# Performance work log

Hardware: AMD Instinct MI355X
Metric: run time of the kernel (lower is better)

## Reference

```python
import jax, jax.numpy as jnp
from jax import lax
import numpy as np

RATE = 6.0          # self.rate buffer
STRIDE = 1
PAD = 1
DIL = 1
R_BLUR = 2          # gaussian blur radius for sigma=1.0 (5x5 kernel)


def _unit_circle():
    # 3x3 kernel taps: center (0,0), 8 outer taps normalized to the unit circle. (y, x) order.
    pts = []
    for ky in (-1.0, 0.0, 1.0):
        for kx in (-1.0, 0.0, 1.0):
            n = np.hypot(ky, kx)
            pts.append([ky / n, kx / n] if n > 0 else [0.0, 0.0])
    return jnp.asarray(np.array(pts, np.float32))  # (9, 2)

UNIT_CIRCLE = _unit_circle()


def blur2d_sphere(x, sigma):
    # Isotropic gaussian blur, depthwise, SAME padding. Kernel values depend on traced sigma.
    c = jnp.arange(-R_BLUR, R_BLUR + 1, dtype=x.dtype)
    g = jnp.exp(-(c[:, None] ** 2 + c[None, :] ** 2) / (2.0 * sigma * sigma))
    g = g / g.sum()
    C = x.shape[1]
    k = jnp.broadcast_to(g[None, None], (C, 1, 2 * R_BLUR + 1, 2 * R_BLUR + 1))
    return lax.conv_general_dilated(x, k, (1, 1), [(R_BLUR, R_BLUR)] * 2,
                                    feature_group_count=C)


def _axis_sample(x, pos, axis, size):
    # 1D linear interpolation gather along `axis` at fractional positions `pos`;
    # out-of-range corners contribute zero (deform_conv semantics).
    dt = x.dtype
    p0 = jnp.floor(pos)
    t = (pos - p0).astype(dt)
    i0 = p0.astype(jnp.int32)
    i1 = i0 + 1
    w0 = (1.0 - t) * ((i0 >= 0) & (i0 < size)).astype(dt)
    w1 = t * ((i1 >= 0) & (i1 < size)).astype(dt)
    g0 = jnp.take(x, jnp.clip(i0, 0, size - 1), axis=axis)
    g1 = jnp.take(x, jnp.clip(i1, 0, size - 1), axis=axis)
    sh = [1, 1, 1, 1]
    sh[axis] = -1
    return w0.reshape(sh) * g0 + w1.reshape(sh) * g1


def _forward(x, sigma, weight):
    x = blur2d_sphere(x, sigma)
    B, C, H, W = x.shape
    O = weight.shape[0]
    off = UNIT_CIRCLE.astype(x.dtype) * (sigma * RATE)  # (9, 2): per-tap (dy, dx), constant over b,h,w
    Ho = (H + 2 * PAD - DIL * 2 - 1) // STRIDE + 1
    Wo = (W + 2 * PAD - DIL * 2 - 1) // STRIDE + 1
    base_y = jnp.arange(Ho, dtype=x.dtype) * STRIDE - PAD
    base_x = jnp.arange(Wo, dtype=x.dtype) * STRIDE - PAD
    wflat = weight.reshape(O, C, 9)
    out = jnp.zeros((B, O, Ho, Wo), x.dtype)
    # Offsets are spatially constant, so deformable bilinear sampling is separable per tap.
    for ky in range(3):
        for kx in range(3):
            k = ky * 3 + kx
            py = base_y + (ky * DIL) + off[k, 0]   # (Ho,)
            px = base_x + (kx * DIL) + off[k, 1]   # (Wo,)
            xr = _axis_sample(x, py, 2, H)          # (B, C, Ho, W)
            v = _axis_sample(xr, px, 3, W)          # (B, C, Ho, Wo)
            out = out + jnp.einsum('bchw,oc->bohw', v, wflat[:, :, k])
    return out


def setup_inputs() -> dict:
    key = jax.random.key(0)
    k1, k2 = jax.random.split(key)
    x = jax.random.normal(k1, (16, 32, 256, 256), jnp.float32)
    fan_in = 32 * 9
    fan_out = 32 * 9
    limit = float(np.sqrt(6.0 / (fan_in + fan_out)))  # xavier_uniform
    weight = jax.random.uniform(k2, (32, 32, 3, 3), jnp.float32, -limit, limit)
    sigma = jnp.float32(1.0)
    return {"x": x, "sigma": sigma, "weight": weight}


def reference(x, sigma, weight):
    return _forward(x, sigma, weight)
```

## Files before the change

kernel.cpp:

```cpp
#include <hip/hip_runtime.h>
#include <math.h>

#define BB 16
#define CC 32
#define OO 32
#define HH 256
#define WW 256
#define HW (HH * WW)
#define PD 8
#define HP (HH + 2 * PD)
#define WP (WW + 2 * PD)
#define NEMAX 36

#define WROWS 30
#define WCOLS 80
#define PLANE (WROWS * WCOLS + 1)

typedef __attribute__((ext_vector_type(8))) short bf16x8;
typedef __attribute__((ext_vector_type(4))) float f32x4;
typedef __attribute__((ext_vector_type(4))) unsigned short us4;
typedef __attribute__((ext_vector_type(8))) unsigned short us8;

__device__ __forceinline__ unsigned short f2bf(float f) {
    unsigned u = __float_as_uint(f);
    u += 0x7fffu + ((u >> 16) & 1u);
    return (unsigned short)(u >> 16);
}
__device__ __forceinline__ float bf2f(unsigned short v) {
    return __uint_as_float((unsigned)v << 16);
}

__global__ __launch_bounds__(256) void blur_t_kernel(const float* __restrict__ x,
                                                     const float* __restrict__ sigma_p,
                                                     unsigned short* __restrict__ xbt) {
    __shared__ __align__(16) unsigned short vb[16][4][264];
    const int t   = threadIdx.x;
    const int blk = ((blockIdx.x & 7) << 7) + (blockIdx.x >> 3);
    const int band = blk & 63;
    const int b    = blk >> 6;
    const int h0   = band << 2;

    const float sigma = sigma_p[0];
    const float inv2s2 = 1.0f / (2.0f * sigma * sigma);
    float e[5], s = 0.0f;
#pragma unroll
    for (int i = 0; i < 5; ++i) {
        float d = (float)(i - 2);
        e[i] = expf(-(d * d) * inv2s2);
        s += e[i];
    }
    const float inv_s = 1.0f / s;
    float wn[5];
#pragma unroll
    for (int i = 0; i < 5; ++i) wn[i] = e[i] * inv_s;

    unsigned short* xb_img = xbt + (size_t)b * (HP * WP * CC);

    const us8 z8 = {0, 0, 0, 0, 0, 0, 0, 0};
    {
        const int j  = t >> 6;
        const int px = (t >> 2) & 15;
        const int ch = t & 3;
        const int xx = (px < PD) ? px : px + WW;
        *reinterpret_cast<us8*>(xb_img + ((size_t)(h0 + PD + j) * WP + xx) * CC + ch * 8) = z8;
    }
    if (h0 < PD) {
#pragma unroll
        for (int j2 = 0; j2 < 4; ++j2) {
            unsigned short* dst = xb_img + (size_t)(h0 + j2) * WP * CC;
            for (int i = t; i < (WP * CC) / 8; i += 256)
                *reinterpret_cast<us8*>(dst + i * 8) = z8;
        }
    }
    if (h0 + 4 > HH - PD) {
#pragma unroll
        for (int j2 = 0; j2 < 4; ++j2) {
            unsigned short* dst = xb_img + (size_t)(h0 + j2 + 2 * PD) * WP * CC;
            for (int i = t; i < (WP * CC) / 8; i += 256)
                *reinterpret_cast<us8*>(dst + i * 8) = z8;
        }
    }

    const int g  = t & 63;
    const int cs = t >> 6;

#pragma unroll
    for (int pass = 0; pass < 2; ++pass) {
        if (pass) __syncthreads();

        {
            const int c15 = t >> 4;
            const int j   = (t >> 2) & 3;
            const int e_  = t & 3;
            const int idx = (e_ < 2) ? (2 + e_) : (258 + e_);
            vb[c15][j][idx] = 0;
        }

#pragma unroll
        for (int it = 0; it < 4; ++it) {
            const int c = (pass << 4) + (it << 2) + cs;
            const float* xc = x + ((size_t)(b * CC + c) * HH) * WW + 4 * g;
            f32x4 v[8];
#pragma unroll
            for (int k = 0; k < 8; ++k) {
                const int r = h0 - 2 + k;
                v[k] = (r >= 0 && r < HH)
                     ? __builtin_nontemporal_load(reinterpret_cast<const f32x4*>(xc + r * WW))
                     : (f32x4){0.f, 0.f, 0.f, 0.f};
            }
#pragma unroll
            for (int j = 0; j < 4; ++j) {
                f32x4 a = {0.f, 0.f, 0.f, 0.f};
#pragma unroll
                for (int i = 0; i < 5; ++i) {
                    a[0] = fmaf(wn[i], v[j + i][0], a[0]);
                    a[1] = fmaf(wn[i], v[j + i][1], a[1]);
                    a[2] = fmaf(wn[i], v[j + i][2], a[2]);
                    a[3] = fmaf(wn[i], v[j + i][3], a[3]);
                }
                us4 bv;
                bv[0] = f2bf(a[0]); bv[1] = f2bf(a[1]);
                bv[2] = f2bf(a[2]); bv[3] = f2bf(a[3]);
                *reinterpret_cast<us4*>(&vb[c & 15][j][4 + 4 * g]) = bv;
            }
        }
        __syncthreads();

        const int cu8 = t & 1;
        const int p4  = (t >> 1) & 63;
        const int jh  = t >> 7;
        const int P   = p4 << 2;
        const int cl0 = cu8 << 3;

#pragma unroll
        for (int jj = 0; jj < 2; ++jj) {
            const int j = (jh << 1) + jj;
            us8 o[4];
#pragma unroll
            for (int cc = 0; cc < 8; ++cc) {
                const unsigned short* vp = &vb[cl0 + cc][j][P];
                us4 r0 = *reinterpret_cast<const us4*>(vp);
                us4 r1 = *reinterpret_cast<const us4*>(vp + 4);
                us4 r2 = *reinterpret_cast<const us4*>(vp + 8);
                float v[12];
#pragma unroll
                for (int q = 0; q < 4; ++q) {
                    v[q]     = bf2f(r0[q]);
                    v[4 + q] = bf2f(r1[q]);
                    v[8 + q] = bf2f(r2[q]);
                }
#pragma unroll
                for (int d = 0; d < 4; ++d) {
                    float a = 0.0f;
#pragma unroll
                    for (int i = 0; i < 5; ++i) a = fmaf(wn[i], v[d + 2 + i], a);
                    o[d][cc] = f2bf(a);
                }
            }
            unsigned short* obj = xb_img + ((size_t)(h0 + PD + j) * WP + PD + P) * CC
                                         + (pass << 4) + cl0;
#pragma unroll
            for (int d = 0; d < 4; ++d)
                *reinterpret_cast<us8*>(obj + d * CC) = o[d];
        }
    }
}

__global__ void wtrans_kernel(const float* __restrict__ wgt,
                              const float* __restrict__ sigma_p,
                              int* __restrict__ meta,
                              unsigned short* __restrict__ wb2) {
    __shared__ int   s_tap[36];
    __shared__ float s_w[36];
    __shared__ int   s_soff[36];
    __shared__ int   s_wrel[36];
    __shared__ int   s_n;
    const int t = threadIdx.x;

    if (t == 0) {
        const float UY[9] = {-0.70710678f, -1.0f, -0.70710678f, 0.0f, 0.0f, 0.0f,
                              0.70710678f,  1.0f,  0.70710678f};
        const float UX[9] = {-0.70710678f, 0.0f, 0.70710678f, -1.0f, 0.0f, 1.0f,
                             -0.70710678f, 0.0f, 0.70710678f};
        const int KYI[9] = {-1, -1, -1, 0, 0, 0, 1, 1, 1};
        const int KXI[9] = {-1, 0, 1, -1, 0, 1, -1, 0, 1};
        const float s6 = sigma_p[0] * 6.0f;
        int n = 0, ok = 1;
        for (int s_ = 0; s_ < 9; ++s_) {
            float offy = UY[s_] * s6, offx = UX[s_] * s6;
            float fy = floorf(offy), fx = floorf(offx);
            float ty = offy - fy,    tx = offx - fx;
            int sy = KYI[s_] + (int)fy;
            int sx = KXI[s_] + (int)fx;
            float wy[2] = {1.0f - ty, ty};
            float wx[2] = {1.0f - tx, tx};
            for (int dy = 0; dy < 2; ++dy)
                for (int dx = 0; dx < 2; ++dx) {
                    float wc = wy[dy] * wx[dx];
                    if (wc != 0.0f) {
                        const int syc = sy + dy, sxc = sx + dx;
                        s_tap[n]  = s_;
                        s_w[n]    = wc;
                        s_soff[n] = (syc * WP + sxc) * CC;
                        s_wrel[n] = (syc + 7) * WCOLS + (sxc + 8);
                        if (syc < -7 || syc > 7 || sxc < -7 || sxc > 7) ok = 0;
                        ++n;
                    }
                }
        }
        for (int i = 1; i < n; ++i) {
            int ks = s_soff[i]; int kt = s_tap[i]; float kw = s_w[i]; int kr = s_wrel[i];
            int j = i - 1;
            while (j >= 0 && s_soff[j] > ks) {
                s_soff[j + 1] = s_soff[j]; s_tap[j + 1] = s_tap[j];
                s_w[j + 1] = s_w[j];       s_wrel[j + 1] = s_wrel[j];
                --j;
            }
            s_soff[j + 1] = ks; s_tap[j + 1] = kt; s_w[j + 1] = kw; s_wrel[j + 1] = kr;
        }
        if (blockIdx.x == 0) {
            meta[0] = n;
            for (int i = 0; i < n; ++i) { meta[1 + i] = s_soff[i]; meta[37 + i] = s_wrel[i]; }
            meta[74] = ok;
        }
        s_n = n;
    }
    __syncthreads();

    const int e = blockIdx.x;
    if (e >= s_n) return;
    for (int i = t; i < 1024; i += 256) {
        int j  = i & 7;
        int l  = (i >> 3) & 63;
        int nh = (i >> 9) & 1;
        int o  = nh * 16 + (l & 15);
        int c  = ((l >> 4) << 3) + j;
        wb2[e * 1024 + i] = f2bf(s_w[e] * wgt[(o * CC + c) * 9 + s_tap[e]]);
    }
}

__global__ __launch_bounds__(512) void mix8_kernel(const unsigned short* __restrict__ xbt,
                                                   const int* __restrict__ meta,
                                                   const unsigned short* __restrict__ wb2,
                                                   float* __restrict__ out) {
    __shared__ bf16x8 win[4 * PLANE];
    const int t    = threadIdx.x;
    const int lane = t & 63;
    const int wv   = t >> 6;
    const int blk  = ((blockIdx.x & 7) << 7) + (blockIdx.x >> 3);
    const int xs   = blk & 3;
    const int band = (blk >> 2) & 15;
    const int b    = blk >> 6;
    const int h0   = band << 4;
    const int x0   = xs << 6;
    const int mrow = lane & 15;
    const int cu   = lane >> 4;
    const int ncorn = meta[0];
    const int ok    = meta[74];

    const unsigned short* img = xbt + (size_t)b * (HP * WP * CC);

    f32x4 acc[8][2];
#pragma unroll
    for (int q = 0; q < 8; ++q) {
        acc[q][0] = (f32x4){0.f, 0.f, 0.f, 0.f};
        acc[q][1] = (f32x4){0.f, 0.f, 0.f, 0.f};
    }

    if (ok) {
        const unsigned short* gsrc = img + ((size_t)(h0 + 1) * WP + x0) * CC;
        for (int i = t; i < WROWS * WCOLS * 4; i += 512) {
            const int cui = i & 3;
            const int pxl = (i >> 2) % WCOLS;
            const int row = (i >> 2) / WCOLS;
            win[cui * PLANE + row * WCOLS + pxl] =
                *reinterpret_cast<const bf16x8*>(gsrc + ((size_t)row * WP + pxl) * CC + cui * 8);
        }
        __syncthreads();

        const int ubase = cu * PLANE + (wv * 2) * WCOLS + mrow;
        for (int e = 0; e < ncorn; ++e) {
            const int ewr = meta[37 + e];
            const bf16x8 b0 = *reinterpret_cast<const bf16x8*>(wb2 + ((e * 2 + 0) * 64 + lane) * 8);
            const bf16x8 b1 = *reinterpret_cast<const bf16x8*>(wb2 + ((e * 2 + 1) * 64 + lane) * 8);
            const int abase = ubase + ewr;
#pragma unroll
            for (int ri = 0; ri < 2; ++ri) {
#pragma unroll
                for (int tx = 0; tx < 4; ++tx) {
                    const bf16x8 a = win[abase + ri * WCOLS + tx * 16];
                    acc[ri * 4 + tx][0] = __builtin_amdgcn_mfma_f32_16x16x32_bf16(a, b0, acc[ri * 4 + tx][0], 0, 0, 0);
                    acc[ri * 4 + tx][1] = __builtin_amdgcn_mfma_f32_16x16x32_bf16(a, b1, acc[ri * 4 + tx][1], 0, 0, 0);
                }
            }
        }
    } else {
        const unsigned short* gb = img + ((size_t)(h0 + wv * 2 + PD) * WP + x0 + PD) * CC
                                       + mrow * CC + cu * 8;
        for (int e = 0; e < ncorn; ++e) {
            const int soff = meta[1 + e];
            const bf16x8 b0 = *reinterpret_cast<const bf16x8*>(wb2 + ((e * 2 + 0) * 64 + lane) * 8);
            const bf16x8 b1 = *reinterpret_cast<const bf16x8*>(wb2 + ((e * 2 + 1) * 64 + lane) * 8);
#pragma unroll
            for (int ri = 0; ri < 2; ++ri) {
#pragma unroll
                for (int tx = 0; tx < 4; ++tx) {
                    const bf16x8 a = *reinterpret_cast<const bf16x8*>(
                        gb + soff + ((size_t)ri * WP + tx * 16) * CC);
                    acc[ri * 4 + tx][0] = __builtin_amdgcn_mfma_f32_16x16x32_bf16(a, b0, acc[ri * 4 + tx][0], 0, 0, 0);
                    acc[ri * 4 + tx][1] = __builtin_amdgcn_mfma_f32_16x16x32_bf16(a, b1, acc[ri * 4 + tx][1], 0, 0, 0);
                }
            }
        }
    }

    const int prow = cu << 2;
    float* op0 = out + ((size_t)b * OO + (lane & 15)) * HW;
#pragma unroll
    for (int ri = 0; ri < 2; ++ri) {
        float* opr = op0 + (size_t)(h0 + wv * 2 + ri) * WW + x0 + prow;
#pragma unroll
        for (int tx = 0; tx < 4; ++tx) {
            *reinterpret_cast<f32x4*>(opr + tx * 16) = acc[ri * 4 + tx][0];
            *reinterpret_cast<f32x4*>(opr + tx * 16 + (size_t)16 * HW) = acc[ri * 4 + tx][1];
        }
    }
}

extern "C" void kernel_launch(void* const* d_in, const int* in_sizes, int n_in,
                              void* d_out, int out_size, void* d_ws, size_t ws_size,
                              hipStream_t stream) {
    const float* x     = (const float*)d_in[0];
    const float* sigma = (const float*)d_in[1];
    const float* wgt   = (const float*)d_in[2];
    float* out = (float*)d_out;

    int* meta           = (int*)d_ws;
    unsigned short* wb2 = (unsigned short*)((char*)d_ws + 512);
    unsigned short* xbt = (unsigned short*)((char*)d_ws + 131072);

    wtrans_kernel<<<36, 256, 0, stream>>>(wgt, sigma, meta, wb2);
    blur_t_kernel<<<BB * 64, 256, 0, stream>>>(x, sigma, xbt);
    mix8_kernel<<<BB * 64, 512, 0, stream>>>(xbt, meta, wb2, out);
}
```

Measured before the change: 156.5 us.

## Fuse blur into the MFMA mixing kernel via shared-memory halo window

Adds a fused kernel that computes the separable 5x5 gaussian blur directly from fp32 input into the shared-memory bf16 window, then runs the MFMA tap accumulation. This skips writing and re-reading the padded bf16 intermediate image in global memory when the offsets fit in the window. The blur is recomputed over halo regions, and the old blur and mix kernels stay as a fallback that exits early on the fast path. The cost is redundant halo blur work and extra launches that return immediately.

```diff
diff --git a/kernel.cpp b/kernel.cpp
--- a/kernel.cpp
+++ b/kernel.cpp
@@ -30,16 +30,7 @@
     return __uint_as_float((unsigned)v << 16);
 }
 
-__global__ __launch_bounds__(256) void blur_t_kernel(const float* __restrict__ x,
-                                                     const float* __restrict__ sigma_p,
-                                                     unsigned short* __restrict__ xbt) {
-    __shared__ __align__(16) unsigned short vb[16][4][264];
-    const int t   = threadIdx.x;
-    const int blk = ((blockIdx.x & 7) << 7) + (blockIdx.x >> 3);
-    const int band = blk & 63;
-    const int b    = blk >> 6;
-    const int h0   = band << 2;
-
+__device__ __forceinline__ void blur_wn(const float* sigma_p, float* wn) {
     const float sigma = sigma_p[0];
     const float inv2s2 = 1.0f / (2.0f * sigma * sigma);
     float e[5], s = 0.0f;
@@ -50,120 +41,8 @@
         s += e[i];
     }
     const float inv_s = 1.0f / s;
-    float wn[5];
 #pragma unroll
     for (int i = 0; i < 5; ++i) wn[i] = e[i] * inv_s;
-
-    unsigned short* xb_img = xbt + (size_t)b * (HP * WP * CC);
-
-    const us8 z8 = {0, 0, 0, 0, 0, 0, 0, 0};
-    {
-        const int j  = t >> 6;
-        const int px = (t >> 2) & 15;
-        const int ch = t & 3;
-        const int xx = (px < PD) ? px : px + WW;
-        *reinterpret_cast<us8*>(xb_img + ((size_t)(h0 + PD + j) * WP + xx) * CC + ch * 8) = z8;
-    }
-    if (h0 < PD) {
-#pragma unroll
-        for (int j2 = 0; j2 < 4; ++j2) {
-            unsigned short* dst = xb_img + (size_t)(h0 + j2) * WP * CC;
-            for (int i = t; i < (WP * CC) / 8; i += 256)
-                *reinterpret_cast<us8*>(dst + i * 8) = z8;
-        }
-    }
-    if (h0 + 4 > HH - PD) {
-#pragma unroll
-        for (int j2 = 0; j2 < 4; ++j2) {
-            unsigned short* dst = xb_img + (size_t)(h0 + j2 + 2 * PD) * WP * CC;
-            for (int i = t; i < (WP * CC) / 8; i += 256)
-                *reinterpret_cast<us8*>(dst + i * 8) = z8;
-        }
-    }
-
-    const int g  = t & 63;
-    const int cs = t >> 6;
-
-#pragma unroll
-    for (int pass = 0; pass < 2; ++pass) {
-        if (pass) __syncthreads();
-
-        {
-            const int c15 = t >> 4;
-            const int j   = (t >> 2) & 3;
-            const int e_  = t & 3;
-            const int idx = (e_ < 2) ? (2 + e_) : (258 + e_);
-            vb[c15][j][idx] = 0;
-        }
-
-#pragma unroll
-        for (int it = 0; it < 4; ++it) {
-            const int c = (pass << 4) + (it << 2) + cs;
-            const float* xc = x + ((size_t)(b * CC + c) * HH) * WW + 4 * g;
-            f32x4 v[8];
-#pragma unroll
-            for (int k = 0; k < 8; ++k) {
-                const int r = h0 - 2 + k;
-                v[k] = (r >= 0 && r < HH)
-                     ? __builtin_nontemporal_load(reinterpret_cast<const f32x4*>(xc + r * WW))
-                     : (f32x4){0.f, 0.f, 0.f, 0.f};
-            }
-#pragma unroll
-            for (int j = 0; j < 4; ++j) {
-                f32x4 a = {0.f, 0.f, 0.f, 0.f};
-#pragma unroll
-                for (int i = 0; i < 5; ++i) {
-                    a[0] = fmaf(wn[i], v[j + i][0], a[0]);
-                    a[1] = fmaf(wn[i], v[j + i][1], a[1]);
-                    a[2] = fmaf(wn[i], v[j + i][2], a[2]);
-                    a[3] = fmaf(wn[i], v[j + i][3], a[3]);
-                }
-                us4 bv;
-                bv[0] = f2bf(a[0]); bv[1] = f2bf(a[1]);
-                bv[2] = f2bf(a[2]); bv[3] = f2bf(a[3]);
-                *reinterpret_cast<us4*>(&vb[c & 15][j][4 + 4 * g]) = bv;
-            }
-        }
-        __syncthreads();
-
-        const int cu8 = t & 1;
-        const int p4  = (t >> 1) & 63;
-        const int jh  = t >> 7;
-        const int P   = p4 << 2;
-        const int cl0 = cu8 << 3;
-
-#pragma unroll
-        for (int jj = 0; jj < 2; ++jj) {
-            const int j = (jh << 1) + jj;
-            us8 o[4];
-#pragma unroll
-            for (int cc = 0; cc < 8; ++cc) {
-                const unsigned short* vp = &vb[cl0 + cc][j][P];
-                us4 r0 = *reinterpret_cast<const us4*>(vp);
-                us4 r1 = *reinterpret_cast<const us4*>(vp + 4);
-                us4 r2 = *reinterpret_cast<const us4*>(vp + 8);
-                float v[12];
-#pragma unroll
-                for (int q = 0; q < 4; ++q) {
-                    v[q]     = bf2f(r0[q]);
-                    v[4 + q] = bf2f(r1[q]);
-                    v[8 + q] = bf2f(r2[q]);
-                }
-#pragma unroll
-                for (int d = 0; d < 4; ++d) {
-                    float a = 0.0f;
-#pragma unroll
-                    for (int i = 0; i < 5; ++i) a = fmaf(wn[i], v[d + 2 + i], a);
-                    o[d][cc] = f2bf(a);
-                }
-            }
-            unsigned short* obj = xb_img + ((size_t)(h0 + PD + j) * WP + PD + P) * CC
-                                         + (pass << 4) + cl0;
-#pragma unroll
-            for (int d = 0; d < 4; ++d)
-                *reinterpret_cast<us8*>(obj + d * CC) = o[d];
-        }
-    }
 }
 
 __global__ void wtrans_kernel(const float* __restrict__ wgt,
@@ -239,11 +118,263 @@
     }
 }
 
-__global__ __launch_bounds__(512) void mix8_kernel(const unsigned short* __restrict__ xbt,
-                                                   const int* __restrict__ meta,
-                                                   const unsigned short* __restrict__ wb2,
-                                                   float* __restrict__ out) {
+__global__ __launch_bounds__(512) void fused_kernel(const float* __restrict__ x,
+                                                    const float* __restrict__ sigma_p,
+                                                    const int* __restrict__ meta,
+                                                    const unsigned short* __restrict__ wb2,
+                                                    float* __restrict__ out) {
     __shared__ bf16x8 win[4 * PLANE];
+    if (!meta[74]) return;
+
+    const int t    = threadIdx.x;
+    const int lane = t & 63;
+    const int wv   = t >> 6;
+    const int blk  = ((blockIdx.x & 7) << 7) + (blockIdx.x >> 3);
+    const int xs   = blk & 3;
+    const int band = (blk >> 2) & 15;
+    const int b    = blk >> 6;
+    const int h0   = band << 4;
+    const int x0   = xs << 6;
+
+    float wn[5];
+    blur_wn(sigma_p, wn);
+
+    for (int tile = t; tile < 1920; tile += 512) {
+        const int c  = tile & 31;
+        const int q  = tile >> 5;
+        const int pg = q % 10;
+        const int rg = q / 10;
+
+        const int yb = h0 - 9 + rg * 5;
+        const int xa = x0 - 12 + pg * 8;
+        const float* xcp = x + ((size_t)(b * CC + c) * HH) * WW;
+
+        f32x4 a5[5][4];
+#pragma unroll
+        for (int j = 0; j < 5; ++j)
+#pragma unroll
+            for (int i = 0; i < 4; ++i) a5[j][i] = (f32x4){0.f, 0.f, 0.f, 0.f};
+
+#pragma unroll
+        for (int r = 0; r < 9; ++r) {
+            const int y = yb + r;
+            const bool rok = (y >= 0) && (y < HH);
+            const float* rp = xcp + y * WW;
+            f32x4 v[4];
+#pragma unroll
+            for (int i = 0; i < 4; ++i) {
+                const int pxb = xa + 4 * i;
+                v[i] = (rok && pxb >= 0 && pxb <= WW - 4)
+                     ? *reinterpret_cast<const f32x4*>(rp + pxb)
+                     : (f32x4){0.f, 0.f, 0.f, 0.f};
+            }
+            const int jlo = (r - 4 > 0) ? r - 4 : 0;
+            const int jhi = (r < 4) ? r : 4;
+#pragma unroll
+            for (int j = 0; j < 5; ++j) {
+                if (j < jlo || j > jhi) continue;
+                const float w = wn[r - j];
+#pragma unroll
+                for (int i = 0; i < 4; ++i) {
+                    a5[j][i][0] = fmaf(w, v[i][0], a5[j][i][0]);
+                    a5[j][i][1] = fmaf(w, v[i][1], a5[j][i][1]);
+                    a5[j][i][2] = fmaf(w, v[i][2], a5[j][i][2]);
+                    a5[j][i][3] = fmaf(w, v[i][3], a5[j][i][3]);
+                }
+            }
+        }
+
+        unsigned short* wp16 = reinterpret_cast<unsigned short*>(win)
+                             + ((c >> 3) * PLANE + (rg * 5) * WCOLS + pg * 8) * 8 + (c & 7);
+#pragma unroll
+        for (int j = 0; j < 5; ++j) {
+            const int yout = h0 - 7 + rg * 5 + j;
+            const bool row_ok = (yout >= 0) && (yout < HH);
+            float vl[16];
+#pragma unroll
+            for (int k = 0; k < 16; ++k) vl[k] = a5[j][k >> 2][k & 3];
+            unsigned short* wrow = wp16 + j * (WCOLS * 8);
+#pragma unroll
+            for (int d = 0; d < 8; ++d) {
+                const int pxo = x0 - 8 + pg * 8 + d;
+                const bool col_ok = (pxo >= 0) && (pxo < WW);
+                float o = 0.0f;
+#pragma unroll
+                for (int i = 0; i < 5; ++i) o = fmaf(wn[i], vl[2 + d + i], o);
+                wrow[d * 8] = (row_ok && col_ok) ? f2bf(o) : (unsigned short)0;
+            }
+        }
+    }
+    __syncthreads();
+
+    const int mrow = lane & 15;
+    const int cu   = lane >> 4;
+    const int ncorn = meta[0];
+
+    f32x4 acc[8][2];
+#pragma unroll
+    for (int qq = 0; qq < 8; ++qq) {
+        acc[qq][0] = (f32x4){0.f, 0.f, 0.f, 0.f};
+        acc[qq][1] = (f32x4){0.f, 0.f, 0.f, 0.f};
+    }
+
+    const int ubase = cu * PLANE + (wv * 2) * WCOLS + mrow;
+    for (int e = 0; e < ncorn; ++e) {
+        const int ewr = meta[37 + e];
+        const bf16x8 b0 = *reinterpret_cast<const bf16x8*>(wb2 + ((e * 2 + 0) * 64 + lane) * 8);
+        const bf16x8 b1 = *reinterpret_cast<const bf16x8*>(wb2 + ((e * 2 + 1) * 64 + lane) * 8);
+        const int abase = ubase + ewr;
+#pragma unroll
+        for (int ri = 0; ri < 2; ++ri) {
+#pragma unroll
+            for (int tx = 0; tx < 4; ++tx) {
+                const bf16x8 a = win[abase + ri * WCOLS + tx * 16];
+                acc[ri * 4 + tx][0] = __builtin_amdgcn_mfma_f32_16x16x32_bf16(a, b0, acc[ri * 4 + tx][0], 0, 0, 0);
+                acc[ri * 4 + tx][1] = __builtin_amdgcn_mfma_f32_16x16x32_bf16(a, b1, acc[ri * 4 + tx][1], 0, 0, 0);
+            }
+        }
+    }
+
+    const int prow = cu << 2;
+    float* op0 = out + ((size_t)b * OO + (lane & 15)) * HW;
+#pragma unroll
+    for (int ri = 0; ri < 2; ++ri) {
+        float* opr = op0 + (size_t)(h0 + wv * 2 + ri) * WW + x0 + prow;
+#pragma unroll
+        for (int tx = 0; tx < 4; ++tx) {
+            *reinterpret_cast<f32x4*>(opr + tx * 16) = acc[ri * 4 + tx][0];
+            *reinterpret_cast<f32x4*>(opr + tx * 16 + (size_t)16 * HW) = acc[ri * 4 + tx][1];
+        }
+    }
+}
+
+__global__ __launch_bounds__(256) void blur_t_kernel(const float* __restrict__ x,
+                                                     const float* __restrict__ sigma_p,
+                                                     const int* __restrict__ meta,
+                                                     unsigned short* __restrict__ xbt) {
+    if (meta[74]) return;
+    __shared__ __align__(16) unsigned short vb[16][4][264];
+    const int t   = threadIdx.x;
+    const int blk = ((blockIdx.x & 7) << 7) + (blockIdx.x >> 3);
+    const int band = blk & 63;
+    const int b    = blk >> 6;
+    const int h0   = band << 2;
+
+    float wn[5];
+    blur_wn(sigma_p, wn);
+
+    unsigned short* xb_img = xbt + (size_t)b * (HP * WP * CC);
+
+    const us8 z8 = {0, 0, 0, 0, 0, 0, 0, 0};
+    {
+        const int j  = t >> 6;
+        const int px = (t >> 2) & 15;
+        const int ch = t & 3;
+        const int xx = (px < PD) ? px : px + WW;
+        *reinterpret_cast<us8*>(xb_img + ((size_t)(h0 + PD + j) * WP + xx) * CC + ch * 8) = z8;
+    }
+    if (h0 < PD) {
+#pragma unroll
+        for (int j2 = 0; j2 < 4; ++j2) {
+            unsigned short* dst = xb_img + (size_t)(h0 + j2) * WP * CC;
+            for (int i = t; i < (WP * CC) / 8; i += 256)
+                *reinterpret_cast<us8*>(dst + i * 8) = z8;
+        }
+    }
+    if (h0 + 4 > HH - PD) {
+#pragma unroll
+        for (int j2 = 0; j2 < 4; ++j2) {
+            unsigned short* dst = xb_img + (size_t)(h0 + j2 + 2 * PD) * WP * CC;
+            for (int i = t; i < (WP * CC) / 8; i += 256)
+                *reinterpret_cast<us8*>(dst + i * 8) = z8;
+        }
+    }
+
+    const int g  = t & 63;
+    const int cs = t >> 6;
+
+#pragma unroll
+    for (int pass = 0; pass < 2; ++pass) {
+        if (pass) __syncthreads();
+        {
+            const int c15 = t >> 4;
+            const int j   = (t >> 2) & 3;
+            const int e_  = t & 3;
+            const int idx = (e_ < 2) ? (2 + e_) : (258 + e_);
+            vb[c15][j][idx] = 0;
+        }
+#pragma unroll
+        for (int it = 0; it < 4; ++it) {
+            const int c = (pass << 4) + (it << 2) + cs;
+            const float* xc = x + ((size_t)(b * CC + c) * HH) * WW + 4 * g;
+            f32x4 v[8];
+#pragma unroll
+            for (int k = 0; k < 8; ++k) {
+                const int r = h0 - 2 + k;
+                v[k] = (r >= 0 && r < HH)
+                     ? *reinterpret_cast<const f32x4*>(xc + r * WW)
+                     : (f32x4){0.f, 0.f, 0.f, 0.f};
+            }
+#pragma unroll
+            for (int j = 0; j < 4; ++j) {
+                f32x4 a = {0.f, 0.f, 0.f, 0.f};
+#pragma unroll
+                for (int i = 0; i < 5; ++i) {
+                    a[0] = fmaf(wn[i], v[j + i][0], a[0]);
+                    a[1] = fmaf(wn[i], v[j + i][1], a[1]);
+                    a[2] = fmaf(wn[i], v[j + i][2], a[2]);
+                    a[3] = fmaf(wn[i], v[j + i][3], a[3]);
+                }
+                us4 bv;
+                bv[0] = f2bf(a[0]); bv[1] = f2bf(a[1]);
+                bv[2] = f2bf(a[2]); bv[3] = f2bf(a[3]);
+                *reinterpret_cast<us4*>(&vb[c & 15][j][4 + 4 * g]) = bv;
+            }
+        }
+        __syncthreads();
+
+        const int cu8 = t & 1;
+        const int p4  = (t >> 1) & 63;
+        const int jh  = t >> 7;
+        const int P   = p4 << 2;
+        const int cl0 = cu8 << 3;
+#pragma unroll
+        for (int jj = 0; jj < 2; ++jj) {
+            const int j = (jh << 1) + jj;
+            us8 o[4];
+#pragma unroll
+            for (int cc = 0; cc < 8; ++cc) {
+                const unsigned short* vp = &vb[cl0 + cc][j][P];
+                us4 r0 = *reinterpret_cast<const us4*>(vp);
+                us4 r1 = *reinterpret_cast<const us4*>(vp + 4);
+                us4 r2 = *reinterpret_cast<const us4*>(vp + 8);
+                float v[12];
+#pragma unroll
+                for (int q = 0; q < 4; ++q) {
+                    v[q] = bf2f(r0[q]); v[4 + q] = bf2f(r1[q]); v[8 + q] = bf2f(r2[q]);
+                }
+#pragma unroll
+                for (int d = 0; d < 4; ++d) {
+                    float a = 0.0f;
+#pragma unroll
+                    for (int i = 0; i < 5; ++i) a = fmaf(wn[i], v[d + 2 + i], a);
+                    o[d][cc] = f2bf(a);
+                }
+            }
+            unsigned short* obj = xb_img + ((size_t)(h0 + PD + j) * WP + PD + P) * CC
+                                         + (pass << 4) + cl0;
+#pragma unroll
+            for (int d = 0; d < 4; ++d)
+                *reinterpret_cast<us8*>(obj + d * CC) = o[d];
+        }
+    }
+}
+
+__global__ __launch_bounds__(512) void mix_gen_kernel(const unsigned short* __restrict__ xbt,
+                                                      const int* __restrict__ meta,
+                                                      const unsigned short* __restrict__ wb2,
+                                                      float* __restrict__ out) {
+    if (meta[74]) return;
     const int t    = threadIdx.x;
     const int lane = t & 63;
     const int wv   = t >> 6;
@@ -256,7 +387,6 @@
     const int mrow = lane & 15;
     const int cu   = lane >> 4;
     const int ncorn = meta[0];
-    const int ok    = meta[74];
 
     const unsigned short* img = xbt + (size_t)b * (HP * WP * CC);
 
@@ -267,49 +397,20 @@
         acc[q][1] = (f32x4){0.f, 0.f, 0.f, 0.f};
     }
 
-    if (ok) {
-        const unsigned short* gsrc = img + ((size_t)(h0 + 1) * WP + x0) * CC;
-        for (int i = t; i < WROWS * WCOLS * 4; i += 512) {
-            const int cui = i & 3;
-            const int pxl = (i >> 2) % WCOLS;
-            const int row = (i >> 2) / WCOLS;
-            win[cui * PLANE + row * WCOLS + pxl] =
-                *reinterpret_cast<const bf16x8*>(gsrc + ((size_t)row * WP + pxl) * CC + cui * 8);
-        }
-        __syncthreads();
-
-        const int ubase = cu * PLANE + (wv * 2) * WCOLS + mrow;
-        for (int e = 0; e < ncorn; ++e) {
-            const int ewr = meta[37 + e];
-            const bf16x8 b0 = *reinterpret_cast<const bf16x8*>(wb2 + ((e * 2 + 0) * 64 + lane) * 8);
-            const bf16x8 b1 = *reinterpret_cast<const bf16x8*>(wb2 + ((e * 2 + 1) * 64 + lane) * 8);
-            const int abase = ubase + ewr;
-#pragma unroll
-            for (int ri = 0; ri < 2; ++ri) {
-#pragma unroll
-                for (int tx = 0; tx < 4; ++tx) {
-                    const bf16x8 a = win[abase + ri * WCOLS + tx * 16];
-                    acc[ri * 4 + tx][0] = __builtin_amdgcn_mfma_f32_16x16x32_bf16(a, b0, acc[ri * 4 + tx][0], 0, 0, 0);
-                    acc[ri * 4 + tx][1] = __builtin_amdgcn_mfma_f32_16x16x32_bf16(a, b1, acc[ri * 4 + tx][1], 0, 0, 0);
-                }
-            }
-        }
-    } else {
-        const unsigned short* gb = img + ((size_t)(h0 + wv * 2 + PD) * WP + x0 + PD) * CC
-                                       + mrow * CC + cu * 8;
-        for (int e = 0; e < ncorn; ++e) {
-            const int soff = meta[1 + e];
-            const bf16x8 b0 = *reinterpret_cast<const bf16x8*>(wb2 + ((e * 2 + 0) * 64 + lane) * 8);
-            const bf16x8 b1 = *reinterpret_cast<const bf16x8*>(wb2 + ((e * 2 + 1) * 64 + lane) * 8);
-#pragma unroll
-            for (int ri = 0; ri < 2; ++ri) {
-#pragma unroll
-                for (int tx = 0; tx < 4; ++tx) {
-                    const bf16x8 a = *reinterpret_cast<const bf16x8*>(
-                        gb + soff + ((size_t)ri * WP + tx * 16) * CC);
-                    acc[ri * 4 + tx][0] = __builtin_amdgcn_mfma_f32_16x16x32_bf16(a, b0, acc[ri * 4 + tx][0], 0, 0, 0);
-                    acc[ri * 4 + tx][1] = __builtin_amdgcn_mfma_f32_16x16x32_bf16(a, b1, acc[ri * 4 + tx][1], 0, 0, 0);
-                }
+    const unsigned short* gb = img + ((size_t)(h0 + wv * 2 + PD) * WP + x0 + PD) * CC
+                                   + mrow * CC + cu * 8;
+    for (int e = 0; e < ncorn; ++e) {
+        const int soff = meta[1 + e];
+        const bf16x8 b0 = *reinterpret_cast<const bf16x8*>(wb2 + ((e * 2 + 0) * 64 + lane) * 8);
+        const bf16x8 b1 = *reinterpret_cast<const bf16x8*>(wb2 + ((e * 2 + 1) * 64 + lane) * 8);
+#pragma unroll
+        for (int ri = 0; ri < 2; ++ri) {
+#pragma unroll
+            for (int tx = 0; tx < 4; ++tx) {
+                const bf16x8 a = *reinterpret_cast<const bf16x8*>(
+                    gb + soff + ((size_t)ri * WP + tx * 16) * CC);
+                acc[ri * 4 + tx][0] = __builtin_amdgcn_mfma_f32_16x16x32_bf16(a, b0, acc[ri * 4 + tx][0], 0, 0, 0);
+                acc[ri * 4 + tx][1] = __builtin_amdgcn_mfma_f32_16x16x32_bf16(a, b1, acc[ri * 4 + tx][1], 0, 0, 0);
             }
         }
     }
@@ -340,6 +441,7 @@
     unsigned short* xbt = (unsigned short*)((char*)d_ws + 131072);
 
     wtrans_kernel<<<36, 256, 0, stream>>>(wgt, sigma, meta, wb2);
-    blur_t_kernel<<<BB * 64, 256, 0, stream>>>(x, sigma, xbt);
-    mix8_kernel<<<BB * 64, 512, 0, stream>>>(xbt, meta, wb2, out);
-}
+    fused_kernel<<<BB * 64, 512, 0, stream>>>(x, sigma, meta, wb2, out);
+    blur_t_kernel<<<BB * 64, 256, 0, stream>>>(x, sigma, meta, xbt);
+    mix_gen_kernel<<<BB * 64, 512, 0, stream>>>(xbt, meta, wb2, out);
+}
```

Measured after the change: 193.8 us. 23.8% more time.
